# Optimization experiments

Measured on AMD Instinct MI355X. Metric: run time of the kernel, lower is better.

## Reference

```python
import jax, jax.numpy as jnp
import numpy as np

T = 2048           # tokens (single prefill sequence)
HIDDEN = 2048
H = 16             # num heads
D_NOPE = 128
D_ROPE = 64
D_V = 128
KV_LORA = 512
EPS = 1e-6
ROPE_THETA = 10000.0


def setup_inputs() -> dict:
    key = jax.random.key(0)
    ks = jax.random.split(key, 7)
    s = 0.02
    return {
        "positions": jnp.arange(T, dtype=jnp.int64) if jax.config.jax_enable_x64 else jnp.arange(T, dtype=jnp.int32),
        "hidden_states": jax.random.normal(ks[0], (T, HIDDEN), dtype=jnp.float32),
        "w_q": jax.random.normal(ks[1], (HIDDEN, H * (D_NOPE + D_ROPE)), dtype=jnp.float32) * s,
        "w_kv_a": jax.random.normal(ks[2], (HIDDEN, KV_LORA + D_ROPE), dtype=jnp.float32) * s,
        "kv_a_ln_w": jax.random.uniform(ks[3], (KV_LORA,), dtype=jnp.float32, minval=0.5, maxval=1.5),
        "w_kv_b": jax.random.normal(ks[4], (KV_LORA, H * (D_NOPE + D_V)), dtype=jnp.float32) * s,
        "w_o": jax.random.normal(ks[5], (H * D_V, HIDDEN), dtype=jnp.float32) * s,
    }


def _rms_norm(x, w):
    var = jnp.mean(jnp.square(x), axis=-1, keepdims=True)
    return x * jax.lax.rsqrt(var + EPS) * w


def _rope_nonneox(x, positions):
    # x: [..., D_ROPE], GPT-J (interleaved) style rotation
    inv_freq = 1.0 / (ROPE_THETA ** (jnp.arange(0, D_ROPE, 2, dtype=jnp.float32) / D_ROPE))
    freqs = positions.astype(jnp.float32)[:, None] * inv_freq  # [T, D_ROPE//2]
    cos, sin = jnp.cos(freqs), jnp.sin(freqs)
    # broadcast over head dim if present
    while cos.ndim < x.ndim:
        cos, sin = cos[:, None], sin[:, None]
    x1, x2 = x[..., 0::2], x[..., 1::2]
    o1 = x1 * cos - x2 * sin
    o2 = x2 * cos + x1 * sin
    return jnp.stack([o1, o2], axis=-1).reshape(x.shape)


def reference(positions, hidden_states, w_q, w_kv_a, kv_a_ln_w, w_kv_b, w_o):
    scaling = (D_NOPE + D_ROPE) ** -0.5
    # q projection (q_lora_rank is None branch)
    q = (hidden_states @ w_q).reshape(T, H, D_NOPE + D_ROPE)
    q_nope, q_pe = q[..., :D_NOPE], q[..., D_NOPE:]
    # compressed KV latent
    latent = hidden_states @ w_kv_a                 # [T, KV_LORA + D_ROPE]
    kv_a = _rms_norm(latent[:, :KV_LORA], kv_a_ln_w)
    k_pe = latent[:, KV_LORA:]                      # [T, D_ROPE], shared across heads
    # decompress to per-head k_nope and v (kv_b_proj)
    kv = (kv_a @ w_kv_b).reshape(T, H, D_NOPE + D_V)
    k_nope, v = kv[..., :D_NOPE], kv[..., D_NOPE:]
    # non-neox RoPE
    q_pe = _rope_nonneox(q_pe, positions)
    k_pe = _rope_nonneox(k_pe, positions)           # [T, D_ROPE]
    # concat rope parts (k_pe broadcast over heads)
    q_full = jnp.concatenate([q_nope, q_pe], axis=-1)                         # [T,H,192]
    k_full = jnp.concatenate([k_nope, jnp.broadcast_to(k_pe[:, None, :], (T, H, D_ROPE))], axis=-1)
    # causal MHA
    scores = jnp.einsum("qhd,khd->hqk", q_full, k_full) * scaling
    causal = positions[:, None] >= positions[None, :]
    scores = jnp.where(causal[None], scores, -jnp.inf)
    attn = jax.nn.softmax(scores, axis=-1)
    out = jnp.einsum("hqk,khd->qhd", attn, v).reshape(T, H * D_V)
    return out @ w_o
```

## Files before the change

### kernel.cpp

```cpp
#include <hip/hip_runtime.h>
#include <hip/hip_bf16.h>
#include <stdint.h>

#define T_SEQ   2048
#define NHEAD   16
#define NPAD1   3712

typedef short bf16x8  __attribute__((ext_vector_type(8)));
typedef float f32x4   __attribute__((ext_vector_type(4)));
typedef float f32x16  __attribute__((ext_vector_type(16)));

__device__ __forceinline__ unsigned short f2bf(float f) {
  union { float f; uint32_t u; } v; v.f = f;
  uint32_t u = v.u;
  uint32_t r = u + 0x7FFF + ((u >> 16) & 1);
  return (unsigned short)(r >> 16);
}

__device__ __forceinline__ void async16(const void* g, void* l) {
  __builtin_amdgcn_global_load_lds(
      (const __attribute__((address_space(1))) void*)g,
      (__attribute__((address_space(3))) void*)l, 16, 0, 0);
}

__device__ __forceinline__ void tr32(const float* __restrict__ in,
    unsigned short* __restrict__ out, int R, int C, int bx, int by,
    float (*tile)[33], int tid) {
  int r0 = bx * 32, c0 = by * 32;
  int tx = tid & 31, ty = tid >> 5;
  for (int i = 0; i < 4; i++)
    tile[ty + i * 8][tx] = in[(size_t)(r0 + ty + i * 8) * C + c0 + tx];
  __syncthreads();
  for (int i = 0; i < 4; i++) {
    int c = ty + i * 8;
    out[(size_t)(c0 + c) * R + r0 + tx] = f2bf(tile[tx][c]);
  }
}

__global__ __launch_bounds__(256) void prep_kernel(
    const float* __restrict__ hs, const float* __restrict__ w_q,
    const float* __restrict__ w_kv_a, const float* __restrict__ w_kv_b,
    const float* __restrict__ w_o,
    unsigned short* __restrict__ hs_bf, unsigned short* __restrict__ wcat_t,
    unsigned short* __restrict__ wkvb_t, unsigned short* __restrict__ wo_t) {
  __shared__ float tile[32][33];
  int bid = blockIdx.x, tid = threadIdx.x;
  if (bid < 4096) {
    int i = (bid * 256 + tid) * 4;
    float4 v = *(const float4*)(hs + i);
    ushort4 o; o.x = f2bf(v.x); o.y = f2bf(v.y); o.z = f2bf(v.z); o.w = f2bf(v.w);
    *(ushort4*)(hs_bf + i) = o;
  } else if (bid < 4096 + 6144) {
    int l = bid - 4096;
    tr32(w_q, wcat_t, 2048, 3072, l & 63, l >> 6, tile, tid);
  } else if (bid < 4096 + 6144 + 1152) {
    int l = bid - (4096 + 6144);
    tr32(w_kv_a, wcat_t + (size_t)3072 * 2048, 2048, 576, l & 63, l >> 6, tile, tid);
  } else if (bid < 4096 + 6144 + 1152 + 2048) {
    int l = bid - (4096 + 6144 + 1152);
    tr32(w_kv_b, wkvb_t, 512, 4096, l & 15, l >> 4, tile, tid);
  } else if (bid < 4096 + 6144 + 1152 + 2048 + 4096) {
    int l = bid - (4096 + 6144 + 1152 + 2048);
    tr32(w_o, wo_t, 2048, 2048, l & 63, l >> 6, tile, tid);
  } else {
    int l = bid - (4096 + 6144 + 1152 + 2048 + 4096);
    uint4 z = (uint4){0, 0, 0, 0};
    *(uint4*)(wcat_t + (size_t)3648 * 2048 + (size_t)(l * 256 + tid) * 8) = z;
  }
}

template<int TM, int OUT_BF16>
__global__ __launch_bounds__(256) void gemm_bt_kernel(
    const unsigned short* __restrict__ A, const unsigned short* __restrict__ B,
    void* __restrict__ Cv, int M, int N, int K) {
  constexpr int MT = TM / 32;
  __shared__ __align__(16) unsigned short Asm[2][TM * 32];
  __shared__ __align__(16) unsigned short Bsm[2][128 * 32];
  int tid = threadIdx.x, wid = tid >> 6, lane = tid & 63;
  int lrow = lane & 15, lquad = lane >> 4;
  int m0 = blockIdx.x * TM, n0 = blockIdx.y * 128;
  int wm = (wid & 1) * (TM / 2), wn = (wid >> 1) * 64;

  int row_s = tid >> 2, cc_s = tid & 3;
  const unsigned short* Ag0 = A + (size_t)(m0 + row_s) * K + cc_s * 8;
  const unsigned short* Ag1 = A + (size_t)(m0 + row_s + 64) * K + cc_s * 8;
  const unsigned short* Bg0 = B + (size_t)(n0 + row_s) * K + cc_s * 8;
  const unsigned short* Bg1 = B + (size_t)(n0 + row_s + 64) * K + cc_s * 8;

  f32x4 acc[MT][4];
  for (int i = 0; i < MT; i++) for (int j = 0; j < 4; j++) acc[i][j] = (f32x4){0.f,0.f,0.f,0.f};

  async16(Ag0, &Asm[0][tid * 8]);
  if (TM == 128) async16(Ag1, &Asm[0][2048 + tid * 8]);
  async16(Bg0, &Bsm[0][tid * 8]);
  async16(Bg1, &Bsm[0][2048 + tid * 8]);

  int cur = 0;
  for (int k0 = 0; k0 < K; k0 += 32) {
    __syncthreads();
    if (k0 + 32 < K) {
      int nxt = cur ^ 1, kk = k0 + 32;
      async16(Ag0 + kk, &Asm[nxt][tid * 8]);
      if (TM == 128) async16(Ag1 + kk, &Asm[nxt][2048 + tid * 8]);
      async16(Bg0 + kk, &Bsm[nxt][tid * 8]);
      async16(Bg1 + kk, &Bsm[nxt][2048 + tid * 8]);
    }
    const unsigned short* As = Asm[cur];
    const unsigned short* Bs = Bsm[cur];
    bf16x8 af[MT], bfr[4];
    for (int mt = 0; mt < MT; mt++)
      af[mt] = *(const bf16x8*)(As + (wm + mt * 16 + lrow) * 32 + lquad * 8);
    for (int nt = 0; nt < 4; nt++)
      bfr[nt] = *(const bf16x8*)(Bs + (wn + nt * 16 + lrow) * 32 + lquad * 8);
    for (int mt = 0; mt < MT; mt++)
      for (int nt = 0; nt < 4; nt++)
        acc[mt][nt] = __builtin_amdgcn_mfma_f32_16x16x32_bf16(af[mt], bfr[nt], acc[mt][nt], 0, 0, 0);
    cur ^= 1;
  }
  for (int mt = 0; mt < MT; mt++)
    for (int nt = 0; nt < 4; nt++) {
      int row = m0 + wm + mt * 16 + lquad * 4;
      int col = n0 + wn + nt * 16 + lrow;
      for (int r = 0; r < 4; r++) {
        if (OUT_BF16)
          ((unsigned short*)Cv)[(size_t)(row + r) * N + col] = f2bf(acc[mt][nt][r]);
        else
          ((float*)Cv)[(size_t)(row + r) * N + col] = acc[mt][nt][r];
      }
    }
}

__global__ __launch_bounds__(256) void postproc1_kernel(
    const float* __restrict__ q_lat,
    const float* __restrict__ ln_w,
    const int* __restrict__ positions,
    unsigned short* __restrict__ kv_a,
    unsigned short* __restrict__ q_full,
    unsigned short* __restrict__ k_pe)
{
  int t = blockIdx.x, tid = threadIdx.x;
  const float* row = q_lat + (size_t)t * NPAD1;
  const float scaling = 0.07216878364870323f;

  float v0 = row[3072 + tid], v1 = row[3072 + 256 + tid];
  float ss = v0 * v0 + v1 * v1;
  for (int m = 1; m < 64; m <<= 1) ss += __shfl_xor(ss, m, 64);
  __shared__ float red[4];
  if ((tid & 63) == 0) red[tid >> 6] = ss;
  __shared__ float kro[64], cf[32], sf[32];
  float pos = (float)positions[t];
  if (tid < 32) {
    float inv_freq = powf(10000.f, -(float)(2 * tid) / 64.f);
    float c, s; sincosf(pos * inv_freq, &s, &c);
    cf[tid] = c; sf[tid] = s;
    float x1 = row[3584 + 2 * tid], x2 = row[3584 + 2 * tid + 1];
    kro[2 * tid]     = x1 * c - x2 * s;
    kro[2 * tid + 1] = x2 * c + x1 * s;
  }
  __syncthreads();
  float rstd = rsqrtf((red[0] + red[1] + red[2] + red[3]) * (1.f / 512.f) + 1e-6f);
  kv_a[(size_t)t * 512 + tid]       = f2bf(v0 * rstd * ln_w[tid]);
  kv_a[(size_t)t * 512 + 256 + tid] = f2bf(v1 * rstd * ln_w[256 + tid]);
  if (tid < 64) k_pe[(size_t)t * 64 + tid] = f2bf(kro[tid]);

  for (int i = tid; i < NHEAD * 128; i += 256) {
    int h = i >> 7, d = i & 127;
    q_full[((size_t)h * T_SEQ + t) * 192 + d] = f2bf(row[h * 192 + d] * scaling);
  }
  for (int i = tid; i < NHEAD * 32; i += 256) {
    int h = i >> 5, p = i & 31;
    float c = cf[p], s = sf[p];
    float x1 = row[h * 192 + 128 + 2 * p], x2 = row[h * 192 + 128 + 2 * p + 1];
    q_full[((size_t)h * T_SEQ + t) * 192 + 128 + 2 * p]     = f2bf((x1 * c - x2 * s) * scaling);
    q_full[((size_t)h * T_SEQ + t) * 192 + 128 + 2 * p + 1] = f2bf((x2 * c + x1 * s) * scaling);
  }
}

__global__ __launch_bounds__(256) void kvpost_kernel(
    const unsigned short* __restrict__ kv_b,
    const unsigned short* __restrict__ k_pe,
    unsigned short* __restrict__ k_full,
    unsigned short* __restrict__ v_t) {
  __shared__ unsigned short tile[32][41];
  int bid = blockIdx.x, tid = threadIdx.x;
  if (bid < 3072) {
    int idx = bid * 256 + tid;
    int cc = idx % 24, rest = idx / 24;
    int t = rest & (T_SEQ - 1), h = rest >> 11;
    uint4 v = (cc < 16)
        ? *(const uint4*)(kv_b + (size_t)t * 4096 + h * 256 + cc * 8)
        : *(const uint4*)(k_pe + (size_t)t * 64 + (cc - 16) * 8);
    *(uint4*)(k_full + (size_t)idx * 8) = v;
  } else {
    int l = bid - 3072;
    int h = l >> 8, t0 = (l & 63) * 32, d0 = ((l >> 6) & 3) * 32;
    int tx = tid & 31, ty = tid >> 5;
    for (int i = 0; i < 4; i++)
      tile[ty + i * 8][tx] = kv_b[(size_t)(t0 + ty + i * 8) * 4096 + h * 256 + 128 + d0 + tx];
    __syncthreads();
    for (int i = 0; i < 4; i++)
      v_t[((size_t)h * 128 + d0 + ty + i * 8) * T_SEQ + t0 + tx] = tile[tx][ty + i * 8];
  }
}

#define PP 76
__global__ __launch_bounds__(256, 2) void flash_kernel(
    const unsigned short* __restrict__ q_full,
    const unsigned short* __restrict__ k_full,
    const unsigned short* __restrict__ v_t,
    unsigned short* __restrict__ attn_out)
{
  __shared__ __align__(16) unsigned short Ksm[2][1536 * 8];
  __shared__ __align__(16) unsigned short Vsm[1024 * 8];
  __shared__ __align__(16) unsigned short Psm[64 * PP];
  __shared__ float Lred[2][64];
  int h = blockIdx.x;
  int y = blockIdx.y;
  int qb = (y < 16) ? (31 - y) : (y - 16);
  int tid = threadIdx.x, wid = tid >> 6, lane = tid & 63;
  int l31 = lane & 31, l5 = lane >> 5, x7 = l31 & 7;
  int rq = wid & 1, kq = wid >> 1;

  const unsigned short* kh = k_full + (size_t)h * T_SEQ * 192;
  const unsigned short* vh = v_t    + (size_t)h * 128 * T_SEQ;

  int gK[6], gV[4];
  #pragma unroll
  for (int j = 0; j < 6; j++) {
    int s = tid + j * 256, row = s / 24, cm = s - row * 24;
    gK[j] = row * 192 + (cm ^ (row & 7)) * 8;
  }
  #pragma unroll
  for (int j = 0; j < 4; j++) {
    int s = tid + j * 256, d = s >> 3;
    gV[j] = d * T_SEQ + ((s & 7) ^ (d & 7)) * 8;
  }
  int kxo[12];
  #pragma unroll
  for (int kc = 0; kc < 12; kc++)
    kxo[kc] = (kq * 32 + l31) * 192 + ((kc * 2 + l5) ^ x7) * 8;
  int vxb[2];
  #pragma unroll
  for (int ntv = 0; ntv < 2; ntv++) vxb[ntv] = (kq * 64 + ntv * 32 + l31) * 64;

  bf16x8 qf[12];
  {
    const unsigned short* qrow =
        q_full + ((size_t)h * T_SEQ + qb * 64 + rq * 32 + l31) * 192 + l5 * 8;
    #pragma unroll
    for (int kc = 0; kc < 12; kc++) qf[kc] = *(const bf16x8*)(qrow + kc * 16);
  }
  f32x16 oacc[2];
  for (int i = 0; i < 2; i++) oacc[i] = (f32x16)(0.f);
  float lsum[16];
  #pragma unroll
  for (int r = 0; r < 16; r++) lsum[r] = 0.f;
  int rl[16];
  #pragma unroll
  for (int r = 0; r < 16; r++) rl[r] = (r & 3) + 8 * (r >> 2) + 4 * l5;

  #pragma unroll
  for (int j = 0; j < 6; j++) async16(kh + gK[j], &Ksm[0][(tid + j * 256) * 8]);

  int cur = 0;
  for (int kb = 0; kb <= qb; kb++) {
    __syncthreads();
    {
      const unsigned short* vb = vh + kb * 64;
      #pragma unroll
      for (int j = 0; j < 4; j++) async16(vb + gV[j], &Vsm[(tid + j * 256) * 8]);
    }
    const unsigned short* Ks = Ksm[cur];
    f32x16 sacc = (f32x16)(0.f);
    #pragma unroll
    for (int kc = 0; kc < 12; kc++) {
      bf16x8 kf = *(const bf16x8*)(Ks + kxo[kc]);
      sacc = __builtin_amdgcn_mfma_f32_32x32x16_bf16(qf[kc], kf, sacc, 0, 0, 0);
    }
    if (kb == qb) {
      int col_g = kb * 64 + kq * 32 + l31;
      int row_b = qb * 64 + rq * 32;
      #pragma unroll
      for (int r = 0; r < 16; r++)
        if (col_g > row_b + rl[r]) sacc[r] = -1e30f;
    }
    #pragma unroll
    for (int r = 0; r < 16; r++) {
      float p = __expf(sacc[r]);
      sacc[r] = p;
      lsum[r] += p;
    }
    #pragma unroll
    for (int r = 0; r < 16; r++)
      Psm[(rq * 32 + rl[r]) * PP + kq * 32 + l31] = f2bf(sacc[r]);
    __syncthreads();
    if (kb < qb) {
      const unsigned short* kb1 = kh + (size_t)(kb + 1) * 64 * 192;
      #pragma unroll
      for (int j = 0; j < 6; j++) async16(kb1 + gK[j], &Ksm[cur ^ 1][(tid + j * 256) * 8]);
    }
    #pragma unroll
    for (int kc = 0; kc < 4; kc++) {
      bf16x8 pf = *(const bf16x8*)(Psm + (rq * 32 + l31) * PP + kc * 16 + l5 * 8);
      #pragma unroll
      for (int ntv = 0; ntv < 2; ntv++) {
        bf16x8 vf = *(const bf16x8*)(Vsm + vxb[ntv] + ((kc * 2 + l5) ^ x7) * 8);
        oacc[ntv] = __builtin_amdgcn_mfma_f32_32x32x16_bf16(pf, vf, oacc[ntv], 0, 0, 0);
      }
    }
    cur ^= 1;
  }

  #pragma unroll
  for (int r = 0; r < 16; r++) {
    float s = lsum[r];
    s += __shfl_xor(s, 1, 64);
    s += __shfl_xor(s, 2, 64);
    s += __shfl_xor(s, 4, 64);
    s += __shfl_xor(s, 8, 64);
    s += __shfl_xor(s, 16, 64);
    lsum[r] = s;
  }
  if (l31 == 0)
    #pragma unroll
    for (int r = 0; r < 16; r++) Lred[kq][rq * 32 + rl[r]] = lsum[r];
  __syncthreads();
  #pragma unroll
  for (int r = 0; r < 16; r++) {
    int row_l = rq * 32 + rl[r];
    float inv = 1.f / (Lred[0][row_l] + Lred[1][row_l]);
    int row_g = qb * 64 + row_l;
    #pragma unroll
    for (int ntv = 0; ntv < 2; ntv++)
      attn_out[(size_t)row_g * 2048 + h * 128 + kq * 64 + ntv * 32 + l31] =
          f2bf(oacc[ntv][r] * inv);
  }
}

extern "C" void kernel_launch(void* const* d_in, const int* in_sizes, int n_in,
                              void* d_out, int out_size, void* d_ws, size_t ws_size,
                              hipStream_t stream) {
  const int*   positions = (const int*)d_in[0];
  const float* hs     = (const float*)d_in[1];
  const float* w_q    = (const float*)d_in[2];
  const float* w_kv_a = (const float*)d_in[3];
  const float* ln_w   = (const float*)d_in[4];
  const float* w_kv_b = (const float*)d_in[5];
  const float* w_o    = (const float*)d_in[6];
  float* out = (float*)d_out;

  char* ws = (char*)d_ws;
  size_t off = 0;
  auto alloc = [&](size_t bytes) { void* p = ws + off; off += (bytes + 255) & ~(size_t)255; return p; };
  unsigned short* hs_bf   = (unsigned short*)alloc((size_t)2048 * 2048 * 2);
  unsigned short* wcat_t  = (unsigned short*)alloc((size_t)NPAD1 * 2048 * 2);
  float*          q_lat   = (float*)alloc((size_t)2048 * NPAD1 * 4);
  unsigned short* kv_a_bf = (unsigned short*)alloc((size_t)2048 * 512 * 2);
  unsigned short* wkvb_t  = (unsigned short*)alloc((size_t)4096 * 512 * 2);
  unsigned short* kv_b    = (unsigned short*)alloc((size_t)2048 * 4096 * 2);
  unsigned short* q_full  = (unsigned short*)alloc((size_t)NHEAD * 2048 * 192 * 2);
  unsigned short* k_pe    = (unsigned short*)alloc((size_t)2048 * 64 * 2);
  unsigned short* k_full  = (unsigned short*)alloc((size_t)NHEAD * 2048 * 192 * 2);
  unsigned short* v_t     = (unsigned short*)alloc((size_t)NHEAD * 128 * 2048 * 2);
  unsigned short* attn_o  = (unsigned short*)alloc((size_t)2048 * 2048 * 2);
  unsigned short* wo_t    = (unsigned short*)alloc((size_t)2048 * 2048 * 2);

  prep_kernel<<<17600, 256, 0, stream>>>(hs, w_q, w_kv_a, w_kv_b, w_o,
                                         hs_bf, wcat_t, wkvb_t, wo_t);
  gemm_bt_kernel<128, 0><<<dim3(16, 29), 256, 0, stream>>>(hs_bf, wcat_t, q_lat, 2048, NPAD1, 2048);
  postproc1_kernel<<<2048, 256, 0, stream>>>(q_lat, ln_w, positions, kv_a_bf, q_full, k_pe);
  gemm_bt_kernel<128, 1><<<dim3(16, 32), 256, 0, stream>>>(kv_a_bf, wkvb_t, kv_b, 2048, 4096, 512);
  kvpost_kernel<<<7168, 256, 0, stream>>>(kv_b, k_pe, k_full, v_t);
  flash_kernel<<<dim3(16, 32), 256, 0, stream>>>(q_full, k_full, v_t, attn_o);
  gemm_bt_kernel<64, 0><<<dim3(32, 16), 256, 0, stream>>>(attn_o, wo_t, out, 2048, 2048, 2048);
}
```

Measured before the change: 283.8 us.

## Deepen GEMM LDS pipeline to four stages with explicit vmcnt waits and XOR swizzle

The bf16 GEMM kernel moves from a double-buffered LDS pipeline to a four-buffer ring with three tiles prefetched ahead. Explicit s_waitcnt vmcnt counts and raw s_barrier replace the full __syncthreads, so loads stay in flight across iterations. It also XOR-swizzles the 16-byte column chunks in LDS to reduce bank conflicts on fragment reads. This doubles LDS use per block, which may lower occupancy, and the hand-tuned wait counts depend on the compiler emitting exactly the expected number of loads.

```diff
diff --git a/kernel.cpp b/kernel.cpp
--- a/kernel.cpp
+++ b/kernel.cpp
@@ -74,14 +74,16 @@
     const unsigned short* __restrict__ A, const unsigned short* __restrict__ B,
     void* __restrict__ Cv, int M, int N, int K) {
   constexpr int MT = TM / 32;
-  __shared__ __align__(16) unsigned short Asm[2][TM * 32];
-  __shared__ __align__(16) unsigned short Bsm[2][128 * 32];
+  __shared__ __align__(16) unsigned short Asm[4][TM * 32];
+  __shared__ __align__(16) unsigned short Bsm[4][128 * 32];
   int tid = threadIdx.x, wid = tid >> 6, lane = tid & 63;
   int lrow = lane & 15, lquad = lane >> 4;
+  int cswz = (lquad ^ ((lane >> 1) & 3)) * 8;
   int m0 = blockIdx.x * TM, n0 = blockIdx.y * 128;
   int wm = (wid & 1) * (TM / 2), wn = (wid >> 1) * 64;
 
-  int row_s = tid >> 2, cc_s = tid & 3;
+  int row_s = tid >> 2;
+  int cc_s = (tid & 3) ^ ((tid >> 3) & 3);
   const unsigned short* Ag0 = A + (size_t)(m0 + row_s) * K + cc_s * 8;
   const unsigned short* Ag1 = A + (size_t)(m0 + row_s + 64) * K + cc_s * 8;
   const unsigned short* Bg0 = B + (size_t)(n0 + row_s) * K + cc_s * 8;
@@ -90,42 +92,57 @@
   f32x4 acc[MT][4];
   for (int i = 0; i < MT; i++) for (int j = 0; j < 4; j++) acc[i][j] = (f32x4){0.f,0.f,0.f,0.f};
 
-  async16(Ag0, &Asm[0][tid * 8]);
-  if (TM == 128) async16(Ag1, &Asm[0][2048 + tid * 8]);
-  async16(Bg0, &Bsm[0][tid * 8]);
-  async16(Bg1, &Bsm[0][2048 + tid * 8]);
-
-  int cur = 0;
-  for (int k0 = 0; k0 < K; k0 += 32) {
-    __syncthreads();
-    if (k0 + 32 < K) {
-      int nxt = cur ^ 1, kk = k0 + 32;
-      async16(Ag0 + kk, &Asm[nxt][tid * 8]);
-      if (TM == 128) async16(Ag1 + kk, &Asm[nxt][2048 + tid * 8]);
-      async16(Bg0 + kk, &Bsm[nxt][tid * 8]);
-      async16(Bg1 + kk, &Bsm[nxt][2048 + tid * 8]);
-    }
-    const unsigned short* As = Asm[cur];
-    const unsigned short* Bs = Bsm[cur];
+  auto stage = [&](int t, int buf) {
+    int kk = t * 32;
+    async16(Ag0 + kk, &Asm[buf][tid * 8]);
+    if constexpr (TM == 128) async16(Ag1 + kk, &Asm[buf][2048 + tid * 8]);
+    async16(Bg0 + kk, &Bsm[buf][tid * 8]);
+    async16(Bg1 + kk, &Bsm[buf][2048 + tid * 8]);
+  };
+
+  const int ktiles = K >> 5;
+  stage(0, 0); stage(1, 1); stage(2, 2);
+  if constexpr (TM == 128) asm volatile("s_waitcnt vmcnt(8)" ::: "memory");
+  else                     asm volatile("s_waitcnt vmcnt(6)" ::: "memory");
+  __builtin_amdgcn_s_barrier();
+  __builtin_amdgcn_sched_barrier(0);
+
+  for (int t = 0; t < ktiles; ++t) {
+    if (t + 3 < ktiles) stage(t + 3, (t + 3) & 3);
+    __builtin_amdgcn_sched_barrier(0);
+    const unsigned short* As = Asm[t & 3];
+    const unsigned short* Bs = Bsm[t & 3];
     bf16x8 af[MT], bfr[4];
     for (int mt = 0; mt < MT; mt++)
-      af[mt] = *(const bf16x8*)(As + (wm + mt * 16 + lrow) * 32 + lquad * 8);
-    for (int nt = 0; nt < 4; nt++)
-      bfr[nt] = *(const bf16x8*)(Bs + (wn + nt * 16 + lrow) * 32 + lquad * 8);
+      af[mt] = *(const bf16x8*)(As + (wm + mt * 16 + lrow) * 32 + cswz);
+    for (int nf = 0; nf < 4; nf++)
+      bfr[nf] = *(const bf16x8*)(Bs + (wn + nf * 16 + lrow) * 32 + cswz);
     for (int mt = 0; mt < MT; mt++)
-      for (int nt = 0; nt < 4; nt++)
-        acc[mt][nt] = __builtin_amdgcn_mfma_f32_16x16x32_bf16(af[mt], bfr[nt], acc[mt][nt], 0, 0, 0);
-    cur ^= 1;
-  }
+      for (int nf = 0; nf < 4; nf++)
+        acc[mt][nf] = __builtin_amdgcn_mfma_f32_16x16x32_bf16(af[mt], bfr[nf], acc[mt][nf], 0, 0, 0);
+    __builtin_amdgcn_sched_barrier(0);
+    if (t + 3 < ktiles) {
+      if constexpr (TM == 128) asm volatile("s_waitcnt vmcnt(8)" ::: "memory");
+      else                     asm volatile("s_waitcnt vmcnt(6)" ::: "memory");
+    } else if (t + 2 < ktiles) {
+      if constexpr (TM == 128) asm volatile("s_waitcnt vmcnt(4)" ::: "memory");
+      else                     asm volatile("s_waitcnt vmcnt(3)" ::: "memory");
+    } else if (t + 1 < ktiles) {
+      asm volatile("s_waitcnt vmcnt(0)" ::: "memory");
+    }
+    __builtin_amdgcn_s_barrier();
+    __builtin_amdgcn_sched_barrier(0);
+  }
+
   for (int mt = 0; mt < MT; mt++)
-    for (int nt = 0; nt < 4; nt++) {
+    for (int nf = 0; nf < 4; nf++) {
       int row = m0 + wm + mt * 16 + lquad * 4;
-      int col = n0 + wn + nt * 16 + lrow;
+      int col = n0 + wn + nf * 16 + lrow;
       for (int r = 0; r < 4; r++) {
         if (OUT_BF16)
-          ((unsigned short*)Cv)[(size_t)(row + r) * N + col] = f2bf(acc[mt][nt][r]);
+          ((unsigned short*)Cv)[(size_t)(row + r) * N + col] = f2bf(acc[mt][nf][r]);
         else
-          ((float*)Cv)[(size_t)(row + r) * N + col] = acc[mt][nt][r];
+          ((float*)Cv)[(size_t)(row + r) * N + col] = acc[mt][nf][r];
       }
     }
 }
```

New measurement: 284.7 us. No clear change (+0.3%).
